# Performance work log

Measured on AMD Instinct MI355X. Metric: run time of the kernel, lower is better.

The kernel has to match this reference:

```python
import jax, jax.numpy as jnp
import numpy as np

N = 100000
E = 1600000
NIN = 128
NOUT = 128


def setup_inputs() -> dict:
    key = jax.random.key(0)
    k1, k2, k3, k4 = jax.random.split(key, 4)
    x = jax.random.normal(k1, (N, NIN), dtype=jnp.float32)
    edge_index = jax.random.randint(k2, (2, E), 0, N, dtype=jnp.int64)
    edge_attr = jnp.ones((E,), dtype=jnp.float32)  # unused by GCNConv
    # PyG Linear weight is [out, in]; glorot-ish init
    W = jax.random.normal(k3, (NOUT, NIN), dtype=jnp.float32) / np.sqrt(NIN)
    b = jnp.zeros((NOUT,), dtype=jnp.float32)
    return {"x": x, "edge_index": edge_index, "edge_attr": edge_attr, "W": W, "b": b}


def reference(x, edge_index, edge_attr, W, b):
    # PyG GCNConv: add self-loops, symmetric degree normalization,
    # linear transform, scatter-add aggregation at destination, + bias.
    n = x.shape[0]
    loops = jnp.arange(n, dtype=edge_index.dtype)
    src = jnp.concatenate([edge_index[0], loops])  # [E+N]
    dst = jnp.concatenate([edge_index[1], loops])  # [E+N]
    # degree over destination (col) including self-loops, edge weight = 1
    deg = jax.ops.segment_sum(jnp.ones_like(dst, dtype=x.dtype), dst, num_segments=n)
    dinv = jnp.where(deg > 0, jax.lax.rsqrt(deg), 0.0)
    norm = dinv[src] * dinv[dst]  # [E+N]
    h = x @ W.T  # [N, NOUT]
    msg = h[src] * norm[:, None]  # [E+N, NOUT]
    out = jax.ops.segment_sum(msg, dst, num_segments=n)  # [N, NOUT]
    return out + b
```

## Files before the change

kernel.cpp:

```cpp
#include <hip/hip_runtime.h>

#define TPB 256
#define NBLK 256
#define BSH 8

typedef __attribute__((ext_vector_type(4))) float f32x4;
typedef __attribute__((ext_vector_type(8))) short short8;

__device__ __forceinline__ unsigned short f2bf(float f) {
    unsigned u = __float_as_uint(f);
    u = (u + 0x7fffu + ((u >> 16) & 1u)) >> 16;
    return (unsigned short)u;
}
__device__ __forceinline__ float bflo(unsigned u) { return __uint_as_float(u << 16); }
__device__ __forceinline__ float bfhi(unsigned u) { return __uint_as_float(u & 0xffff0000u); }


__global__ __launch_bounds__(256) void k_bhist(const int* __restrict__ dst,
                                               int* __restrict__ blockhist, int E) {
    __shared__ int sh[512];
    int t = threadIdx.x;
    sh[t] = 0; sh[t + 256] = 0;
    __syncthreads();
    int chunk = (E + NBLK - 1) / NBLK;
    int lo = blockIdx.x * chunk;
    int hi = min(E, lo + chunk);
    for (int e = lo + t; e < hi; e += 256)
        atomicAdd(&sh[dst[e] >> BSH], 1);
    __syncthreads();
    int* row = blockhist + blockIdx.x * 512;
    row[t] = sh[t];
    row[t + 256] = sh[t + 256];
}


__global__ __launch_bounds__(512) void k_bscan(int* __restrict__ blockhist,
                                               int* __restrict__ bbase, int E) {
    __shared__ int tmp[2][512];
    int t = threadIdx.x;
    int run = 0;
    for (int b = 0; b < NBLK; ++b) {
        int v = blockhist[b * 512 + t];
        blockhist[b * 512 + t] = run;
        run += v;
    }
    tmp[0][t] = run;
    __syncthreads();
    int sb = 0;
    for (int d = 1; d < 512; d <<= 1) {
        int val = tmp[sb][t] + ((t >= d) ? tmp[sb][t - d] : 0);
        tmp[sb ^ 1][t] = val;
        sb ^= 1;
        __syncthreads();
    }
    bbase[t] = tmp[sb][t] - run;
    if (t == 0) bbase[512] = E;
}


__global__ __launch_bounds__(256) void k_bscatter(const int* __restrict__ src,
                                                  const int* __restrict__ dst,
                                                  const int* __restrict__ blockhist,
                                                  const int* __restrict__ bbase,
                                                  unsigned* __restrict__ packed, int E) {
    __shared__ int sh[512];
    int t = threadIdx.x;
    const int* row = blockhist + blockIdx.x * 512;
    sh[t]       = bbase[t]       + row[t];
    sh[t + 256] = bbase[t + 256] + row[t + 256];
    __syncthreads();
    int chunk = (E + NBLK - 1) / NBLK;
    int lo = blockIdx.x * chunk;
    int hi = min(E, lo + chunk);
    for (int e = lo + t; e < hi; e += 256) {
        int d = dst[e];
        int pos = atomicAdd(&sh[d >> BSH], 1);
        packed[pos] = ((unsigned)src[e] << 8) | (unsigned)(d & 255);
    }
}


__global__ __launch_bounds__(256) void k_bcsr(const unsigned* __restrict__ packed,
                                              const int* __restrict__ bbase,
                                              int* __restrict__ offsets,
                                              int* __restrict__ sorted_src,
                                              float* __restrict__ dinv, int N, int E) {
    __shared__ int hist[256];
    __shared__ int tmp[2][256];
    __shared__ int scur[256];
    int b = blockIdx.x;
    int s0 = bbase[b], s1 = bbase[b + 1];
    int t = threadIdx.x;
    hist[t] = 0;
    __syncthreads();
    for (int e = s0 + t; e < s1; e += 256)
        atomicAdd(&hist[packed[e] & 255u], 1);
    __syncthreads();
    int v = hist[t];
    tmp[0][t] = v;
    __syncthreads();
    int sb = 0;
    for (int d = 1; d < 256; d <<= 1) {
        int val = tmp[sb][t] + ((t >= d) ? tmp[sb][t - d] : 0);
        tmp[sb ^ 1][t] = val;
        sb ^= 1;
        __syncthreads();
    }
    int gbase = s0 + (tmp[sb][t] - v);
    scur[t] = gbase;
    int d = (b << BSH) + t;
    if (d < N) { offsets[d] = gbase; dinv[d] = rsqrtf((float)v + 1.0f); }
    if (b == 0 && t == 0) offsets[N] = E;
    __syncthreads();
    for (int e = s0 + t; e < s1; e += 256) {
        unsigned pk = packed[e];
        int pos = atomicAdd(&scur[pk & 255u], 1);
        sorted_src[pos] = (int)(pk >> 8);
    }
}


__global__ __launch_bounds__(256) void k_gemm(const float* __restrict__ x,
                                              const float* __restrict__ W,
                                              const float* __restrict__ dinv,
                                              unsigned short* __restrict__ g, int n) {
    __shared__ unsigned short wb[128][136];
    const int tid = threadIdx.x;

    for (int chunk = tid; chunk < 2048; chunk += 256) {
        int nrow = chunk >> 4, k8 = (chunk & 15) << 3;
        const float* wp = W + nrow * 128 + k8;
        float4 w0 = *(const float4*)wp;
        float4 w1 = *(const float4*)(wp + 4);
        union { unsigned short u[8]; uint4 q; } pk;
        pk.u[0] = f2bf(w0.x); pk.u[1] = f2bf(w0.y); pk.u[2] = f2bf(w0.z); pk.u[3] = f2bf(w0.w);
        pk.u[4] = f2bf(w1.x); pk.u[5] = f2bf(w1.y); pk.u[6] = f2bf(w1.z); pk.u[7] = f2bf(w1.w);
        *(uint4*)&wb[nrow][k8] = pk.q;
    }
    __syncthreads();

    const int lane = tid & 63;
    const int wid  = tid >> 6;
    const int l15  = lane & 15;
    const int quad = lane >> 4;
    const int row  = blockIdx.x * 64 + wid * 16 + l15;
    const int rowc = (row < n) ? row : (n - 1);

    f32x4 acc[8];
    #pragma unroll
    for (int t = 0; t < 8; ++t) acc[t] = (f32x4){0.f, 0.f, 0.f, 0.f};

    #pragma unroll
    for (int ks = 0; ks < 4; ++ks) {
        const int kb = ks * 32 + quad * 8;
        float4 a0 = *(const float4*)(x + (long)rowc * 128 + kb);
        float4 a1 = *(const float4*)(x + (long)rowc * 128 + kb + 4);
        union { unsigned short u[8]; short8 v; } af;
        af.u[0] = f2bf(a0.x); af.u[1] = f2bf(a0.y); af.u[2] = f2bf(a0.z); af.u[3] = f2bf(a0.w);
        af.u[4] = f2bf(a1.x); af.u[5] = f2bf(a1.y); af.u[6] = f2bf(a1.z); af.u[7] = f2bf(a1.w);
        #pragma unroll
        for (int t = 0; t < 8; ++t) {
            short8 bf = *(const short8*)&wb[t * 16 + l15][kb];
            acc[t] = __builtin_amdgcn_mfma_f32_16x16x32_bf16(af.v, bf, acc[t], 0, 0, 0);
        }
    }

    int   orow[4];
    float dv[4];
    #pragma unroll
    for (int r = 0; r < 4; ++r) {
        orow[r] = blockIdx.x * 64 + wid * 16 + quad * 4 + r;
        dv[r]   = (orow[r] < n) ? dinv[orow[r]] : 0.f;
    }
    #pragma unroll
    for (int t = 0; t < 8; ++t) {
        int col = t * 16 + l15;
        #pragma unroll
        for (int r = 0; r < 4; ++r) {
            if (orow[r] < n)
                g[(long)orow[r] * 128 + col] = f2bf(acc[t][r] * dv[r]);
        }
    }
}


__global__ __launch_bounds__(256) void k_aggregate(const int* __restrict__ sorted_src,
                                                   const int* __restrict__ offsets,
                                                   const unsigned short* __restrict__ g,
                                                   const float* __restrict__ dinv,
                                                   const float* __restrict__ b,
                                                   float* __restrict__ out, int n) {
    int d = blockIdx.x * (TPB / 32) + (threadIdx.x >> 5);
    if (d >= n) return;
    int c = (threadIdx.x & 31) << 2;

    int s0 = offsets[d];
    int s1 = offsets[d + 1];

    float4 acc = make_float4(0.f, 0.f, 0.f, 0.f);
    auto addrow = [&](int r) {
        uint2 p = *(const uint2*)(g + (long)r * 128 + c);
        acc.x += bflo(p.x); acc.y += bfhi(p.x);
        acc.z += bflo(p.y); acc.w += bfhi(p.y);
    };

    addrow(d);
    int e = s0;
    for (; e + 8 <= s1; e += 8) {
        int a[8];
        #pragma unroll
        for (int j = 0; j < 8; ++j) a[j] = sorted_src[e + j];
        #pragma unroll
        for (int j = 0; j < 8; ++j) addrow(a[j]);
    }
    for (; e + 4 <= s1; e += 4) {
        int a[4];
        #pragma unroll
        for (int j = 0; j < 4; ++j) a[j] = sorted_src[e + j];
        #pragma unroll
        for (int j = 0; j < 4; ++j) addrow(a[j]);
    }
    for (; e < s1; ++e) addrow(sorted_src[e]);

    float s = dinv[d];
    float4 bb = *(const float4*)(b + c);
    float4 r = make_float4(acc.x * s + bb.x, acc.y * s + bb.y,
                           acc.z * s + bb.z, acc.w * s + bb.w);
    *(float4*)(out + (long)d * 128 + c) = r;
}


extern "C" void kernel_launch(void* const* d_in, const int* in_sizes, int n_in,
                              void* d_out, int out_size, void* d_ws, size_t ws_size,
                              hipStream_t stream) {
    const float* x  = (const float*)d_in[0];
    const int*   ei = (const int*)d_in[1];
    const float* W  = (const float*)d_in[3];
    const float* b  = (const float*)d_in[4];
    float* out = (float*)d_out;

    const int N = in_sizes[0] / 128;
    const int E = in_sizes[1] / 2;
    const int* src = ei;
    const int* dst = ei + E;
    const int NB = (N + 255) >> BSH;

    char* p = (char*)d_ws;
    auto carve = [&](size_t bytes) { char* q = p; p += (bytes + 255) & ~(size_t)255; return q; };
    int*            blockhist  = (int*)           carve((size_t)NBLK * 512 * 4);
    int*            bbase      = (int*)           carve(513 * 4);
    int*            offsets    = (int*)           carve((size_t)(N + 1) * 4);
    float*          dinv       = (float*)         carve((size_t)N * 4);
    unsigned*       packed     = (unsigned*)      carve((size_t)E * 4);
    int*            sorted_src = (int*)           carve((size_t)E * 4);
    unsigned short* g          = (unsigned short*)carve((size_t)N * 128 * 2);

    k_bhist   <<<NBLK, TPB, 0, stream>>>(dst, blockhist, E);
    k_bscan   <<<1, 512, 0, stream>>>(blockhist, bbase, E);
    k_bscatter<<<NBLK, TPB, 0, stream>>>(src, dst, blockhist, bbase, packed, E);
    k_bcsr    <<<NB, TPB, 0, stream>>>(packed, bbase, offsets, sorted_src, dinv, N, E);

    k_gemm<<<(N + 63) / 64, TPB, 0, stream>>>(x, W, dinv, g, N);

    k_aggregate<<<(N + (TPB / 32) - 1) / (TPB / 32), TPB, 0, stream>>>(
        sorted_src, offsets, g, dinv, b, out, N);
}
```

Measured before the change: 253.6 us.

## Stage bucket CSR writes in LDS, vectorize GEMM stores, batch scan loads

The CSR build kernel now sorts each bucket's source indices in shared memory and writes them out contiguously, falling back to direct scatter when a bucket exceeds capacity. The GEMM swaps MFMA operand order so each lane holds four consecutive columns of one row, which lets it store packed 8-byte bf16 chunks instead of scattered 2-byte stores. The block-scan loop now batches eight loads before its dependent updates. The aims are coalesced global writes and fewer serialized loads, at the cost of 24KB extra LDS in the CSR kernel, which may lower its occupancy.

After: 243.1 us. 1.04x faster.

```diff
diff --git a/kernel.cpp b/kernel.cpp
--- a/kernel.cpp
+++ b/kernel.cpp
@@ -3,6 +3,7 @@
 #define TPB 256
 #define NBLK 256
 #define BSH 8
+#define BCAP 6144
 
 typedef __attribute__((ext_vector_type(4))) float f32x4;
 typedef __attribute__((ext_vector_type(8))) short short8;
@@ -39,10 +40,12 @@
     __shared__ int tmp[2][512];
     int t = threadIdx.x;
     int run = 0;
-    for (int b = 0; b < NBLK; ++b) {
-        int v = blockhist[b * 512 + t];
-        blockhist[b * 512 + t] = run;
-        run += v;
+    for (int b = 0; b < NBLK; b += 8) {
+        int v[8];
+        #pragma unroll
+        for (int j = 0; j < 8; ++j) v[j] = blockhist[(b + j) * 512 + t];
+        #pragma unroll
+        for (int j = 0; j < 8; ++j) { blockhist[(b + j) * 512 + t] = run; run += v[j]; }
     }
     tmp[0][t] = run;
     __syncthreads();
@@ -88,8 +91,10 @@
     __shared__ int hist[256];
     __shared__ int tmp[2][256];
     __shared__ int scur[256];
+    __shared__ unsigned stage[BCAP];
     int b = blockIdx.x;
     int s0 = bbase[b], s1 = bbase[b + 1];
+    int cnt = s1 - s0;
     int t = threadIdx.x;
     hist[t] = 0;
     __syncthreads();
@@ -106,16 +111,27 @@
         sb ^= 1;
         __syncthreads();
     }
-    int gbase = s0 + (tmp[sb][t] - v);
-    scur[t] = gbase;
+    int lbase = tmp[sb][t] - v;
+    scur[t] = lbase;
     int d = (b << BSH) + t;
-    if (d < N) { offsets[d] = gbase; dinv[d] = rsqrtf((float)v + 1.0f); }
+    if (d < N) { offsets[d] = s0 + lbase; dinv[d] = rsqrtf((float)v + 1.0f); }
     if (b == 0 && t == 0) offsets[N] = E;
     __syncthreads();
-    for (int e = s0 + t; e < s1; e += 256) {
-        unsigned pk = packed[e];
-        int pos = atomicAdd(&scur[pk & 255u], 1);
-        sorted_src[pos] = (int)(pk >> 8);
+    if (cnt <= BCAP) {
+        for (int e = s0 + t; e < s1; e += 256) {
+            unsigned pk = packed[e];
+            int pos = atomicAdd(&scur[pk & 255u], 1);
+            stage[pos] = pk >> 8;
+        }
+        __syncthreads();
+        for (int i = t; i < cnt; i += 256)
+            sorted_src[s0 + i] = (int)stage[i];
+    } else {
+        for (int e = s0 + t; e < s1; e += 256) {
+            unsigned pk = packed[e];
+            int pos = atomicAdd(&scur[pk & 255u], 1);
+            sorted_src[(long)s0 + pos] = (int)(pk >> 8);
+        }
     }
 }
 
@@ -161,24 +177,23 @@
         #pragma unroll
         for (int t = 0; t < 8; ++t) {
             short8 bf = *(const short8*)&wb[t * 16 + l15][kb];
-            acc[t] = __builtin_amdgcn_mfma_f32_16x16x32_bf16(af.v, bf, acc[t], 0, 0, 0);
-        }
-    }
-
-    int   orow[4];
-    float dv[4];
-    #pragma unroll
-    for (int r = 0; r < 4; ++r) {
-        orow[r] = blockIdx.x * 64 + wid * 16 + quad * 4 + r;
-        dv[r]   = (orow[r] < n) ? dinv[orow[r]] : 0.f;
-    }
-    #pragma unroll
-    for (int t = 0; t < 8; ++t) {
-        int col = t * 16 + l15;
-        #pragma unroll
-        for (int r = 0; r < 4; ++r) {
-            if (orow[r] < n)
-                g[(long)orow[r] * 128 + col] = f2bf(acc[t][r] * dv[r]);
+            acc[t] = __builtin_amdgcn_mfma_f32_16x16x32_bf16(bf, af.v, acc[t], 0, 0, 0);
+        }
+    }
+
+    if (row < n) {
+        float dv = dinv[row];
+        unsigned short* gp = g + (long)row * 128 + quad * 4;
+        #pragma unroll
+        for (int t = 0; t < 8; ++t) {
+            unsigned short u0 = f2bf(acc[t][0] * dv);
+            unsigned short u1 = f2bf(acc[t][1] * dv);
+            unsigned short u2 = f2bf(acc[t][2] * dv);
+            unsigned short u3 = f2bf(acc[t][3] * dv);
+            uint2 pk;
+            pk.x = (unsigned)u0 | ((unsigned)u1 << 16);
+            pk.y = (unsigned)u2 | ((unsigned)u3 << 16);
+            *(uint2*)(gp + t * 16) = pk;
         }
     }
 }
```
